# Performance work log

Hardware: AMD Instinct MI355X
Metric: run time of the kernel (lower is better)

## Reference

```python
import jax, jax.numpy as jnp
import numpy as np

N = 100000   # nodes
E = 1200000  # edges
D = 64       # dim == num_features
L = 5        # num_gc_layers
G = 128      # num graphs in batch
BN_EPS = 1e-5
NORM_EPS = 1e-12

def setup_inputs() -> dict:
    key = jax.random.key(0)
    ks = jax.random.split(key, 16)
    s = 0.05
    x = jax.random.normal(ks[0], (N, D), jnp.float32)
    edge_index = jax.random.randint(ks[1], (2, E), 0, N, dtype=jnp.int32)
    batch = jnp.sort(jax.random.randint(ks[2], (N,), 0, G, dtype=jnp.int32))
    # Encoder_support: Linear(D, D)
    Ws = jax.random.normal(ks[3], (D, D), jnp.float32) * s
    bs = jnp.zeros((D,), jnp.float32)
    # GIN MLPs per layer: Linear(D,D) -> ReLU -> Linear(D,D)
    W1 = jax.random.normal(ks[4], (L, D, D), jnp.float32) * s
    b1 = jnp.zeros((L, D), jnp.float32)
    W2 = jax.random.normal(ks[5], (L, D, D), jnp.float32) * s
    b2 = jnp.zeros((L, D), jnp.float32)
    # BatchNorm affine params
    bn_gamma = jnp.ones((L, D), jnp.float32)
    bn_beta = jnp.zeros((L, D), jnp.float32)
    # proj_head: Linear(L*D, L*D) -> ReLU -> Linear(L*D, L*D)
    Wp1 = jax.random.normal(ks[6], (L * D, L * D), jnp.float32) * s
    bp1 = jnp.zeros((L * D,), jnp.float32)
    Wp2 = jax.random.normal(ks[7], (L * D, L * D), jnp.float32) * s
    bp2 = jnp.zeros((L * D,), jnp.float32)
    return {"x": x, "edge_index": edge_index, "batch": batch,
            "Ws": Ws, "bs": bs, "W1": W1, "b1": b1, "W2": W2, "b2": b2,
            "bn_gamma": bn_gamma, "bn_beta": bn_beta,
            "Wp1": Wp1, "bp1": bp1, "Wp2": Wp2, "bp2": bp2}

def _l2norm(v):
    # F.normalize(v, dim=1): v / max(||v||_2, 1e-12)
    n = jnp.sqrt(jnp.sum(v * v, axis=1, keepdims=True))
    return v / jnp.maximum(n, NORM_EPS)

def reference(x, edge_index, batch, Ws, bs, W1, b1, W2, b2,
              bn_gamma, bn_beta, Wp1, bp1, Wp2, bp2):
    src, dst = edge_index[0], edge_index[1]
    h = x @ Ws + bs  # Encoder_support
    xs = []
    for i in range(L):
        # GINConv (eps=0): nn(x + sum_{j->i} x_j)
        agg = jax.ops.segment_sum(h[src], dst, num_segments=N)  # [N, D]
        z = h + agg
        z = jnp.maximum(z @ W1[i] + b1[i], 0.0) @ W2[i] + b2[i]
        z = jnp.maximum(z, 0.0)  # F.relu after conv
        # BatchNorm1d (training-mode batch stats over nodes)
        mean = jnp.mean(z, axis=0)
        var = jnp.var(z, axis=0)
        h = bn_gamma[i] * (z - mean) * jax.lax.rsqrt(var + BN_EPS) + bn_beta[i]
        xs.append(h)
    # global_add_pool per layer, concat along feature dim -> [G, L*D]
    pooled = jnp.concatenate(
        [jax.ops.segment_sum(h_, batch, num_segments=G) for h_ in xs], axis=1)
    y = jnp.maximum(pooled @ Wp1 + bp1, 0.0) @ Wp2 + bp2
    return (_l2norm(y), _l2norm(pooled))
```

## Files before the change

kernel.cpp:

```cpp
#include <hip/hip_runtime.h>
#include <hip/hip_bf16.h>
#include <hip/hip_fp16.h>

constexpr int Nn = 100000;
constexpr int Ee = 1200000;
constexpr int Ll = 5;
constexpr int Gg = 128;
constexpr int PDim = 320;

constexpr int NB    = 98;
constexpr int BCAP  = 16384;
constexpr int CHUNK = 4096;
constexpr int NBLK_A = (Ee + CHUNK - 1) / CHUNK;

typedef short short8 __attribute__((ext_vector_type(8)));
typedef float f32x4 __attribute__((ext_vector_type(4)));

union U4S8 { uint4 u; short8 s; };

__device__ inline ushort f2bf(float f) {
    const uint u = __float_as_uint(f);
    return (ushort)((u + 0x7fffu + ((u >> 16) & 1u)) >> 16);
}
__device__ inline uint pack2(float lo, float hi) {
    return (uint)f2bf(lo) | ((uint)f2bf(hi) << 16);
}
__device__ inline ushort f2h(float f) {
    const __half h = __float2half(f);
    return *(const ushort*)&h;
}
__device__ inline uint pack2h(float lo, float hi) {
    return (uint)f2h(lo) | ((uint)f2h(hi) << 16);
}
__device__ inline float h2f_lo(uint u) {
    const ushort s = (ushort)(u & 0xffffu);
    return __half2float(*(const __half*)&s);
}
__device__ inline float h2f_hi(uint u) {
    const ushort s = (ushort)(u >> 16);
    return __half2float(*(const __half*)&s);
}
__device__ inline void split2(float x0, float x1, uint& hi, uint& lo) {
    const ushort h0 = f2bf(x0), h1 = f2bf(x1);
    hi = (uint)h0 | ((uint)h1 << 16);
    const float r0 = x0 - __uint_as_float((uint)h0 << 16);
    const float r1 = x1 - __uint_as_float((uint)h1 << 16);
    lo = pack2(r0, r1);
}

__device__ inline int lower_bound_i(const int* __restrict__ a, int n, int v)
{
    int lo = 0, hi = n;
    while (lo < hi) {
        const int m = (lo + hi) >> 1;
        if (a[m] < v) lo = m + 1; else hi = m;
    }
    return lo;
}

__global__ __launch_bounds__(256) void conv_weights(
    const float* __restrict__ Ws, const float* __restrict__ W1,
    const float* __restrict__ W2, ushort* __restrict__ WThi,
    ushort* __restrict__ WTlo)
{
    const int m = blockIdx.x;
    const float* src = (m == 0) ? Ws
                     : (m <= 5) ? W1 + (size_t)(m - 1) * 4096
                                : W2 + (size_t)(m - 6) * 4096;
    ushort* dh = WThi + (size_t)m * 4096;
    ushort* dl = WTlo + (size_t)m * 4096;
    const int t = threadIdx.x;
    const int col = t & 63;
    const int k0 = (t >> 6) * 16;
    #pragma unroll
    for (int i = 0; i < 16; i++) {
        const int k = k0 + i;
        const float w = src[k * 64 + col];
        const ushort h = f2bf(w);
        dh[col * 64 + k] = h;
        dl[col * 64 + k] = f2bf(w - __uint_as_float((uint)h << 16));
    }
}

__global__ __launch_bounds__(256) void gemm_enc(
    const float* __restrict__ A1,
    const ushort* __restrict__ WThi, const ushort* __restrict__ WTlo,
    const float* __restrict__ bias, ushort* __restrict__ Ys)
{
    const int t = threadIdx.x;
    const int w = t >> 6;
    const int l = t & 63;
    const int lr = l & 15;
    const int lk = l >> 4;

    short8 bHi[4][2], bLo[4][2];
    #pragma unroll
    for (int nt = 0; nt < 4; nt++)
        #pragma unroll
        for (int c = 0; c < 2; c++) {
            const int off = (nt * 16 + lr) * 64 + c * 32 + lk * 8;
            U4S8 uh, ul;
            uh.u = *(const uint4*)(WThi + off);
            ul.u = *(const uint4*)(WTlo + off);
            bHi[nt][c] = uh.s;
            bLo[nt][c] = ul.s;
        }

    const int arow = blockIdx.x * 64 + w * 16 + lr;
    short8 aHi[2], aLo[2];
    if (arow < Nn) {
        #pragma unroll
        for (int c = 0; c < 2; c++) {
            const float* p1 = A1 + (size_t)arow * 64 + c * 32 + lk * 8;
            const float4 v0 = *(const float4*)p1;
            const float4 v1 = *(const float4*)(p1 + 4);
            U4S8 rh, rl;
            uint* ph = (uint*)&rh.u;
            uint* pl = (uint*)&rl.u;
            split2(v0.x, v0.y, ph[0], pl[0]);
            split2(v0.z, v0.w, ph[1], pl[1]);
            split2(v1.x, v1.y, ph[2], pl[2]);
            split2(v1.z, v1.w, ph[3], pl[3]);
            aHi[c] = rh.s;
            aLo[c] = rl.s;
        }
    } else {
        U4S8 z; z.u = make_uint4(0, 0, 0, 0);
        aHi[0] = aHi[1] = z.s;
        aLo[0] = aLo[1] = z.s;
    }

    f32x4 acc[4] = {};
    #pragma unroll
    for (int nt = 0; nt < 4; nt++)
        #pragma unroll
        for (int c = 0; c < 2; c++) {
            acc[nt] = __builtin_amdgcn_mfma_f32_16x16x32_bf16(
                aLo[c], bHi[nt][c], acc[nt], 0, 0, 0);
            acc[nt] = __builtin_amdgcn_mfma_f32_16x16x32_bf16(
                aHi[c], bLo[nt][c], acc[nt], 0, 0, 0);
            acc[nt] = __builtin_amdgcn_mfma_f32_16x16x32_bf16(
                aHi[c], bHi[nt][c], acc[nt], 0, 0, 0);
        }

    #pragma unroll
    for (int nt = 0; nt < 4; nt++) {
        const int ccol = nt * 16 + lr;
        const float bb = bias[ccol];
        #pragma unroll
        for (int j = 0; j < 4; j++) {
            const int crow = blockIdx.x * 64 + w * 16 + lk * 4 + j;
            if (crow < Nn)
                Ys[(size_t)crow * 64 + ccol] = f2h(acc[nt][j] + bb);
        }
    }
}

__global__ __launch_bounds__(256) void fused_mlp(
    const float* __restrict__ Uf,
    const ushort* __restrict__ WT1hi, const ushort* __restrict__ WT1lo,
    const float* __restrict__ b1v,
    const ushort* __restrict__ WT2hi, const ushort* __restrict__ WT2lo,
    const float* __restrict__ b2v,
    float* __restrict__ Z, float* __restrict__ stats)
{
    const int t = threadIdx.x;
    const int w = t >> 6;
    const int l = t & 63;
    const int lr = l & 15;
    const int lk = l >> 4;

    __shared__ ushort Mhi[64][72];
    __shared__ ushort Mlo[64][72];
    __shared__ float red[2][4][4][16];

    short8 b1Hi[4][2], b1Lo[4][2];
    #pragma unroll
    for (int nt = 0; nt < 4; nt++)
        #pragma unroll
        for (int c = 0; c < 2; c++) {
            const int off = (nt * 16 + lr) * 64 + c * 32 + lk * 8;
            U4S8 uh, ul;
            uh.u = *(const uint4*)(WT1hi + off);
            ul.u = *(const uint4*)(WT1lo + off);
            b1Hi[nt][c] = uh.s;
            b1Lo[nt][c] = ul.s;
        }

    const int arow = blockIdx.x * 64 + w * 16 + lr;
    short8 aHi[2], aLo[2];
    if (arow < Nn) {
        #pragma unroll
        for (int c = 0; c < 2; c++) {
            const float* p1 = Uf + (size_t)arow * 64 + c * 32 + lk * 8;
            const float4 v0 = *(const float4*)p1;
            const float4 v1 = *(const float4*)(p1 + 4);
            U4S8 rh, rl;
            uint* ph = (uint*)&rh.u;
            uint* pl = (uint*)&rl.u;
            split2(v0.x, v0.y, ph[0], pl[0]);
            split2(v0.z, v0.w, ph[1], pl[1]);
            split2(v1.x, v1.y, ph[2], pl[2]);
            split2(v1.z, v1.w, ph[3], pl[3]);
            aHi[c] = rh.s;
            aLo[c] = rl.s;
        }
    } else {
        U4S8 z; z.u = make_uint4(0, 0, 0, 0);
        aHi[0] = aHi[1] = z.s;
        aLo[0] = aLo[1] = z.s;
    }

    f32x4 acc[4] = {};
    #pragma unroll
    for (int nt = 0; nt < 4; nt++)
        #pragma unroll
        for (int c = 0; c < 2; c++) {
            acc[nt] = __builtin_amdgcn_mfma_f32_16x16x32_bf16(
                aLo[c], b1Hi[nt][c], acc[nt], 0, 0, 0);
            acc[nt] = __builtin_amdgcn_mfma_f32_16x16x32_bf16(
                aHi[c], b1Lo[nt][c], acc[nt], 0, 0, 0);
            acc[nt] = __builtin_amdgcn_mfma_f32_16x16x32_bf16(
                aHi[c], b1Hi[nt][c], acc[nt], 0, 0, 0);
        }

    #pragma unroll
    for (int nt = 0; nt < 4; nt++) {
        const int ccol = nt * 16 + lr;
        const float bb = b1v[ccol];
        #pragma unroll
        for (int j = 0; j < 4; j++) {
            const int rloc = w * 16 + lk * 4 + j;
            const float m = fmaxf(acc[nt][j] + bb, 0.f);
            const ushort h = f2bf(m);
            Mhi[rloc][ccol] = h;
            Mlo[rloc][ccol] = f2bf(m - __uint_as_float((uint)h << 16));
        }
    }
    __syncthreads();

    short8 b2Hi[4][2], b2Lo[4][2];
    #pragma unroll
    for (int nt = 0; nt < 4; nt++)
        #pragma unroll
        for (int c = 0; c < 2; c++) {
            const int off = (nt * 16 + lr) * 64 + c * 32 + lk * 8;
            U4S8 uh, ul;
            uh.u = *(const uint4*)(WT2hi + off);
            ul.u = *(const uint4*)(WT2lo + off);
            b2Hi[nt][c] = uh.s;
            b2Lo[nt][c] = ul.s;
        }

    short8 a2Hi[2], a2Lo[2];
    #pragma unroll
    for (int c = 0; c < 2; c++) {
        U4S8 uh, ul;
        uh.u = *(const uint4*)&Mhi[w * 16 + lr][c * 32 + lk * 8];
        ul.u = *(const uint4*)&Mlo[w * 16 + lr][c * 32 + lk * 8];
        a2Hi[c] = uh.s;
        a2Lo[c] = ul.s;
    }

    f32x4 acc2[4] = {};
    #pragma unroll
    for (int nt = 0; nt < 4; nt++)
        #pragma unroll
        for (int c = 0; c < 2; c++) {
            acc2[nt] = __builtin_amdgcn_mfma_f32_16x16x32_bf16(
                a2Lo[c], b2Hi[nt][c], acc2[nt], 0, 0, 0);
            acc2[nt] = __builtin_amdgcn_mfma_f32_16x16x32_bf16(
                a2Hi[c], b2Lo[nt][c], acc2[nt], 0, 0, 0);
            acc2[nt] = __builtin_amdgcn_mfma_f32_16x16x32_bf16(
                a2Hi[c], b2Hi[nt][c], acc2[nt], 0, 0, 0);
        }

    float s[4], s2[4];
    #pragma unroll
    for (int nt = 0; nt < 4; nt++) {
        const int ccol = nt * 16 + lr;
        const float bb = b2v[ccol];
        s[nt] = 0.f; s2[nt] = 0.f;
        #pragma unroll
        for (int j = 0; j < 4; j++) {
            const int crow = blockIdx.x * 64 + w * 16 + lk * 4 + j;
            if (crow < Nn) {
                const float v = fmaxf(acc2[nt][j] + bb, 0.f);
                Z[(size_t)crow * 64 + ccol] = v;
                s[nt] += v; s2[nt] += v * v;
            }
        }
    }

    #pragma unroll
    for (int nt = 0; nt < 4; nt++) {
        s[nt]  += __shfl_xor(s[nt], 16);  s[nt]  += __shfl_xor(s[nt], 32);
        s2[nt] += __shfl_xor(s2[nt], 16); s2[nt] += __shfl_xor(s2[nt], 32);
    }
    if (l < 16) {
        #pragma unroll
        for (int nt = 0; nt < 4; nt++) {
            red[0][w][nt][l] = s[nt];
            red[1][w][nt][l] = s2[nt];
        }
    }
    __syncthreads();
    if (t < 64) {
        float ts = 0.f, ts2 = 0.f;
        #pragma unroll
        for (int wv = 0; wv < 4; wv++) {
            ts  += red[0][wv][t >> 4][t & 15];
            ts2 += red[1][wv][t >> 4][t & 15];
        }
        atomicAdd(&stats[t], ts);
        atomicAdd(&stats[64 + t], ts2);
    }
}

__global__ void init_csr(int* __restrict__ gCursor)
{
    const int t = threadIdx.x;
    if (t < NB) gCursor[t] = t * BCAP;
}

__global__ __launch_bounds__(256) void bin_edges(
    const int* __restrict__ ei, int* __restrict__ gCursor,
    uint2* __restrict__ binned)
{
    __shared__ int hist[NB];
    __shared__ int base[NB];
    __shared__ int cur[NB];
    const int t = threadIdx.x;
    const int e0 = blockIdx.x * CHUNK;
    const int eEnd = min(e0 + CHUNK, Ee);
    if (t < NB) hist[t] = 0;
    __syncthreads();
    for (int e = e0 + t; e < eEnd; e += 256)
        atomicAdd(&hist[ei[Ee + e] >> 10], 1);
    __syncthreads();
    if (t < NB) {
        base[t] = atomicAdd(&gCursor[t], hist[t]);
        cur[t] = 0;
    }
    __syncthreads();
    for (int e = e0 + t; e < eEnd; e += 256) {
        const int s = ei[e];
        const int d = ei[Ee + e];
        const int b = d >> 10;
        const int pos = atomicAdd(&cur[b], 1);
        binned[(size_t)base[b] + pos] = make_uint2((uint)d, (uint)s);
    }
}

__global__ __launch_bounds__(128) void scan_buckets(
    const int* __restrict__ gCursor, int* __restrict__ bucketBase)
{
    __shared__ int sh[128];
    const int t = threadIdx.x;
    const int c = (t < NB) ? gCursor[t] - t * BCAP : 0;
    sh[t] = c;
    __syncthreads();
    for (int off = 1; off < 128; off <<= 1) {
        const int u = (t >= off) ? sh[t - off] : 0;
        __syncthreads();
        sh[t] += u;
        __syncthreads();
    }
    bucketBase[t] = sh[t] - c;
}

__global__ __launch_bounds__(256) void build_csr(
    const uint2* __restrict__ binned, const int* __restrict__ gCursor,
    const int* __restrict__ bucketBase, int* __restrict__ rowptr,
    int* __restrict__ colidx)
{
    __shared__ int degS[1024];
    __shared__ int sh[256];
    __shared__ int colStage[BCAP];
    const int b = blockIdx.x;
    const int t = threadIdx.x;
    const int cnt = gCursor[b] - b * BCAP;
    const int base = bucketBase[b];
    const uint2* src = binned + (size_t)b * BCAP;

    for (int i = t; i < 1024; i += 256) degS[i] = 0;
    __syncthreads();
    for (int i = t; i < cnt; i += 256)
        atomicAdd(&degS[src[i].x & 1023], 1);
    __syncthreads();

    const int b4 = t * 4;
    const int v0 = degS[b4], v1 = degS[b4 + 1], v2 = degS[b4 + 2], v3 = degS[b4 + 3];
    const int sSum = v0 + v1 + v2 + v3;
    sh[t] = sSum;
    __syncthreads();
    for (int off = 1; off < 256; off <<= 1) {
        const int u = (t >= off) ? sh[t - off] : 0;
        __syncthreads();
        sh[t] += u;
        __syncthreads();
    }
    const int excl = sh[t] - sSum;
    const int p0 = excl, p1 = excl + v0, p2 = excl + v0 + v1, p3 = excl + v0 + v1 + v2;

    const int grow = b * 1024 + b4;
    if (grow + 3 <= Nn) {
        *(int4*)(rowptr + grow) = make_int4(base + p0, base + p1, base + p2, base + p3);
    } else {
        if (grow + 0 <= Nn) rowptr[grow + 0] = base + p0;
        if (grow + 1 <= Nn) rowptr[grow + 1] = base + p1;
        if (grow + 2 <= Nn) rowptr[grow + 2] = base + p2;
        if (grow + 3 <= Nn) rowptr[grow + 3] = base + p3;
    }

    degS[b4] = p0; degS[b4 + 1] = p1; degS[b4 + 2] = p2; degS[b4 + 3] = p3;
    __syncthreads();
    for (int i = t; i < cnt; i += 256) {
        const uint2 p = src[i];
        const int pos = atomicAdd(&degS[p.x & 1023], 1);
        colStage[pos] = (int)p.y;
    }
    __syncthreads();
    for (int i = t; i < cnt; i += 256) colidx[base + i] = colStage[i];
}

__global__ __launch_bounds__(256) void gather_agg_inc(
    const int* __restrict__ rowptr, const int* __restrict__ col,
    const ushort* __restrict__ hs, float* __restrict__ u)
{
    const int r = blockIdx.x * 32 + (threadIdx.x >> 3);
    const int q = threadIdx.x & 7;
    const int beg = rowptr[r], end = rowptr[r + 1];
    float a[8];
    {
        const uint4 v = *(const uint4*)(hs + (size_t)r * 64 + q * 8);
        a[0] = h2f_lo(v.x); a[1] = h2f_hi(v.x);
        a[2] = h2f_lo(v.y); a[3] = h2f_hi(v.y);
        a[4] = h2f_lo(v.z); a[5] = h2f_hi(v.z);
        a[6] = h2f_lo(v.w); a[7] = h2f_hi(v.w);
    }
    for (int j = beg; j < end; j++) {
        const int s = col[j];
        const uint4 v = *(const uint4*)(hs + (size_t)s * 64 + q * 8);
        a[0] += h2f_lo(v.x); a[1] += h2f_hi(v.x);
        a[2] += h2f_lo(v.y); a[3] += h2f_hi(v.y);
        a[4] += h2f_lo(v.z); a[5] += h2f_hi(v.z);
        a[6] += h2f_lo(v.w); a[7] += h2f_hi(v.w);
    }
    float* o = u + (size_t)r * 64 + q * 8;
    *(float4*)o       = make_float4(a[0], a[1], a[2], a[3]);
    *(float4*)(o + 4) = make_float4(a[4], a[5], a[6], a[7]);
}

__global__ void bn_finalize(
    float* __restrict__ stats, const float* __restrict__ gamma,
    const float* __restrict__ beta, float* __restrict__ sc, int layer)
{
    const int c = threadIdx.x;
    const float mean = stats[c] * (1.0f / Nn);
    const float var = stats[64 + c] * (1.0f / Nn) - mean * mean;
    const float scale = gamma[layer * 64 + c] * rsqrtf(var + 1e-5f);
    sc[c] = scale;
    sc[64 + c] = beta[layer * 64 + c] - mean * scale;
    stats[c] = 0.f;
    stats[64 + c] = 0.f;
}

__global__ __launch_bounds__(256) void bn_apply_pool(
    const float* __restrict__ z, ushort* __restrict__ hs,
    const int* __restrict__ batch, const float* __restrict__ sc,
    float* __restrict__ pooled, int layer)
{
    const int g = blockIdx.x >> 3;
    const int sub = blockIdx.x & 7;
    const int lo = lower_bound_i(batch, Nn, g);
    const int hi = lower_bound_i(batch, Nn, g + 1);
    const int t = threadIdx.x;
    const int cq = t & 15;
    const int rg = (t >> 4) + sub * 16;
    float scl[4], sft[4], acc[4] = {};
    #pragma unroll
    for (int i = 0; i < 4; i++) {
        scl[i] = sc[cq * 4 + i];
        sft[i] = sc[64 + cq * 4 + i];
    }
    for (int row = lo + rg; row < hi; row += 128) {
        const float4 v = *(const float4*)(z + (size_t)row * 64 + cq * 4);
        const float a0 = fmaf(scl[0], v.x, sft[0]);
        const float a1 = fmaf(scl[1], v.y, sft[1]);
        const float a2 = fmaf(scl[2], v.z, sft[2]);
        const float a3 = fmaf(scl[3], v.w, sft[3]);
        uint2 p;
        p.x = pack2h(a0, a1);
        p.y = pack2h(a2, a3);
        *(uint2*)(hs + (size_t)row * 64 + cq * 4) = p;
        acc[0] += a0; acc[1] += a1; acc[2] += a2; acc[3] += a3;
    }
    __shared__ float red[16][16][4];
    #pragma unroll
    for (int i = 0; i < 4; i++) red[t >> 4][cq][i] = acc[i];
    __syncthreads();
    if (t < 64) {
        const int c2 = t >> 2, j = t & 3;
        float s = 0.f;
        #pragma unroll
        for (int r = 0; r < 16; r++) s += red[r][c2][j];
        atomicAdd(&pooled[g * PDim + layer * 64 + c2 * 4 + j], s);
    }
}

template<bool RELU>
__global__ __launch_bounds__(256) void proj(
    const float* __restrict__ X, const float* __restrict__ W,
    const float* __restrict__ bias, float* __restrict__ Y)
{
    const int idx = blockIdx.x * 256 + threadIdx.x;
    const int r = idx / PDim;
    const int c = idx - r * PDim;
    float acc = bias[c];
    #pragma unroll 8
    for (int k = 0; k < PDim; k++)
        acc = fmaf(X[r * PDim + k], W[k * PDim + c], acc);
    if constexpr (RELU) acc = fmaxf(acc, 0.f);
    Y[idx] = acc;
}

__global__ __launch_bounds__(64) void l2norm_rows(
    const float* __restrict__ X, float* __restrict__ out)
{
    const int r = blockIdx.x;
    const int l = threadIdx.x;
    float v[5];
    float s = 0.f;
    #pragma unroll
    for (int i = 0; i < 5; i++) {
        v[i] = X[r * PDim + i * 64 + l];
        s += v[i] * v[i];
    }
    #pragma unroll
    for (int off = 32; off > 0; off >>= 1) s += __shfl_down(s, off);
    s = __shfl(s, 0);
    const float d = fmaxf(sqrtf(s), 1e-12f);
    #pragma unroll
    for (int i = 0; i < 5; i++)
        out[r * PDim + i * 64 + l] = v[i] / d;
}

extern "C" void kernel_launch(void* const* d_in, const int* in_sizes, int n_in,
                              void* d_out, int out_size, void* d_ws, size_t ws_size,
                              hipStream_t stream)
{
    const float* x     = (const float*)d_in[0];
    const int*   ei    = (const int*)d_in[1];
    const int*   batch = (const int*)d_in[2];
    const float* Ws    = (const float*)d_in[3];
    const float* bs    = (const float*)d_in[4];
    const float* W1    = (const float*)d_in[5];
    const float* b1    = (const float*)d_in[6];
    const float* W2    = (const float*)d_in[7];
    const float* b2    = (const float*)d_in[8];
    const float* gamma = (const float*)d_in[9];
    const float* beta  = (const float*)d_in[10];
    const float* Wp1   = (const float*)d_in[11];
    const float* bp1   = (const float*)d_in[12];
    const float* Wp2   = (const float*)d_in[13];
    const float* bp2   = (const float*)d_in[14];
    float* out = (float*)d_out;

    float*  Uf  = (float*)d_ws;
    float*  Zf  = Uf + (size_t)Nn * 64;
    ushort* Hs  = (ushort*)(Zf + (size_t)Nn * 64);
    ushort* WThi = Hs + (size_t)Nn * 64;
    ushort* WTlo = WThi + 11 * 4096;
    float* pooled = (float*)(WTlo + 11 * 4096);
    float* ytmp   = pooled + (size_t)Gg * PDim;
    float* ypro   = ytmp + (size_t)Gg * PDim;
    float* stats  = ypro + (size_t)Gg * PDim;
    float* sc     = stats + 128;
    int* rowptr = (int*)(sc + 128);
    int* colidx = rowptr + Nn + 1;
    int* gCursor = colidx + Ee;
    int* bucketBase = gCursor + 128;
    size_t woff = (size_t)((bucketBase + 128) - (int*)d_ws);
    woff = (woff + 1) & ~(size_t)1;
    uint2* binned = (uint2*)((int*)d_ws + woff);

    const int gemmGrid = (Nn + 63) / 64;

    hipMemsetAsync(stats, 0, 128 * sizeof(float), stream);
    hipMemsetAsync(pooled, 0, (size_t)Gg * PDim * sizeof(float), stream);

    conv_weights<<<11, 256, 0, stream>>>(Ws, W1, W2, WThi, WTlo);

    init_csr<<<1, 128, 0, stream>>>(gCursor);
    bin_edges<<<NBLK_A, 256, 0, stream>>>(ei, gCursor, binned);
    scan_buckets<<<1, 128, 0, stream>>>(gCursor, bucketBase);
    build_csr<<<NB, 256, 0, stream>>>(binned, gCursor, bucketBase, rowptr, colidx);

    gemm_enc<<<gemmGrid, 256, 0, stream>>>(x, WThi, WTlo, bs, Hs);

    for (int l = 0; l < Ll; l++) {
        gather_agg_inc<<<Nn / 32, 256, 0, stream>>>(rowptr, colidx, Hs, Uf);
        fused_mlp<<<gemmGrid, 256, 0, stream>>>(
            Uf,
            WThi + (size_t)(1 + l) * 4096, WTlo + (size_t)(1 + l) * 4096,
            b1 + (size_t)l * 64,
            WThi + (size_t)(6 + l) * 4096, WTlo + (size_t)(6 + l) * 4096,
            b2 + (size_t)l * 64,
            Zf, stats);
        bn_finalize<<<1, 64, 0, stream>>>(stats, gamma, beta, sc, l);
        bn_apply_pool<<<Gg * 8, 256, 0, stream>>>(Zf, Hs, batch, sc, pooled, l);
    }

    proj<true><<<160, 256, 0, stream>>>(pooled, Wp1, bp1, ytmp);
    proj<false><<<160, 256, 0, stream>>>(ytmp, Wp2, bp2, ypro);

    l2norm_rows<<<Gg, 64, 0, stream>>>(ypro, out);
    l2norm_rows<<<Gg, 64, 0, stream>>>(pooled, out + Gg * PDim);
}
```

Baseline: 668.2 us.

## Fold BatchNorm affine into gather and pooling; store intermediates as fp16

The BatchNorm affine is pushed through the linear aggregation: the gather kernel now reads raw fp16 Z, sums the neighbours, then applies scale*sum + (deg+1)*shift. Pooling sums raw Z per graph and applies the affine once at the end, using per-graph node counts. This removes the separate bn_apply pass and its write of normalized features. The aggregated input U and the MLP output Z are stored as fp16 instead of fp32, and the hidden MLP activation goes through a single fp16 shared buffer. Together these roughly halve the activation traffic, at the cost of some fp16 precision loss.

```diff
diff --git a/kernel.cpp b/kernel.cpp
--- a/kernel.cpp
+++ b/kernel.cpp
@@ -56,6 +56,19 @@
         if (a[m] < v) lo = m + 1; else hi = m;
     }
     return lo;
+}
+
+__global__ void init_csr(const int* __restrict__ batch, int* __restrict__ gCursor,
+                         int* __restrict__ cnt, float* __restrict__ sc)
+{
+    const int t = threadIdx.x;
+    if (t < NB) gCursor[t] = t * BCAP;
+    {
+        const int lo = lower_bound_i(batch, Nn, t);
+        const int hi = lower_bound_i(batch, Nn, t + 1);
+        cnt[t] = hi - lo;
+    }
+    if (t < 64) { sc[t] = 1.f; sc[64 + t] = 0.f; }
 }
 
 __global__ __launch_bounds__(256) void conv_weights(
@@ -157,12 +170,12 @@
 }
 
 __global__ __launch_bounds__(256) void fused_mlp(
-    const float* __restrict__ Uf,
+    const ushort* __restrict__ Us,
     const ushort* __restrict__ WT1hi, const ushort* __restrict__ WT1lo,
     const float* __restrict__ b1v,
     const ushort* __restrict__ WT2hi, const ushort* __restrict__ WT2lo,
     const float* __restrict__ b2v,
-    float* __restrict__ Z, float* __restrict__ stats)
+    ushort* __restrict__ Zs, float* __restrict__ stats)
 {
     const int t = threadIdx.x;
     const int w = t >> 6;
@@ -170,8 +183,7 @@
     const int lr = l & 15;
     const int lk = l >> 4;
 
-    __shared__ ushort Mhi[64][72];
-    __shared__ ushort Mlo[64][72];
+    __shared__ ushort Mh[64][72];
     __shared__ float red[2][4][4][16];
 
     short8 b1Hi[4][2], b1Lo[4][2];
@@ -192,16 +204,14 @@
     if (arow < Nn) {
         #pragma unroll
         for (int c = 0; c < 2; c++) {
-            const float* p1 = Uf + (size_t)arow * 64 + c * 32 + lk * 8;
-            const float4 v0 = *(const float4*)p1;
-            const float4 v1 = *(const float4*)(p1 + 4);
+            const uint4 v = *(const uint4*)(Us + (size_t)arow * 64 + c * 32 + lk * 8);
             U4S8 rh, rl;
             uint* ph = (uint*)&rh.u;
             uint* pl = (uint*)&rl.u;
-            split2(v0.x, v0.y, ph[0], pl[0]);
-            split2(v0.z, v0.w, ph[1], pl[1]);
-            split2(v1.x, v1.y, ph[2], pl[2]);
-            split2(v1.z, v1.w, ph[3], pl[3]);
+            split2(h2f_lo(v.x), h2f_hi(v.x), ph[0], pl[0]);
+            split2(h2f_lo(v.y), h2f_hi(v.y), ph[1], pl[1]);
+            split2(h2f_lo(v.z), h2f_hi(v.z), ph[2], pl[2]);
+            split2(h2f_lo(v.w), h2f_hi(v.w), ph[3], pl[3]);
             aHi[c] = rh.s;
             aLo[c] = rl.s;
         }
@@ -231,10 +241,7 @@
         #pragma unroll
         for (int j = 0; j < 4; j++) {
             const int rloc = w * 16 + lk * 4 + j;
-            const float m = fmaxf(acc[nt][j] + bb, 0.f);
-            const ushort h = f2bf(m);
-            Mhi[rloc][ccol] = h;
-            Mlo[rloc][ccol] = f2bf(m - __uint_as_float((uint)h << 16));
+            Mh[rloc][ccol] = f2h(fmaxf(acc[nt][j] + bb, 0.f));
         }
     }
     __syncthreads();
@@ -255,11 +262,16 @@
     short8 a2Hi[2], a2Lo[2];
     #pragma unroll
     for (int c = 0; c < 2; c++) {
-        U4S8 uh, ul;
-        uh.u = *(const uint4*)&Mhi[w * 16 + lr][c * 32 + lk * 8];
-        ul.u = *(const uint4*)&Mlo[w * 16 + lr][c * 32 + lk * 8];
-        a2Hi[c] = uh.s;
-        a2Lo[c] = ul.s;
+        const uint4 v = *(const uint4*)&Mh[w * 16 + lr][c * 32 + lk * 8];
+        U4S8 rh, rl;
+        uint* ph = (uint*)&rh.u;
+        uint* pl = (uint*)&rl.u;
+        split2(h2f_lo(v.x), h2f_hi(v.x), ph[0], pl[0]);
+        split2(h2f_lo(v.y), h2f_hi(v.y), ph[1], pl[1]);
+        split2(h2f_lo(v.z), h2f_hi(v.z), ph[2], pl[2]);
+        split2(h2f_lo(v.w), h2f_hi(v.w), ph[3], pl[3]);
+        a2Hi[c] = rh.s;
+        a2Lo[c] = rl.s;
     }
 
     f32x4 acc2[4] = {};
@@ -286,7 +298,7 @@
             const int crow = blockIdx.x * 64 + w * 16 + lk * 4 + j;
             if (crow < Nn) {
                 const float v = fmaxf(acc2[nt][j] + bb, 0.f);
-                Z[(size_t)crow * 64 + ccol] = v;
+                Zs[(size_t)crow * 64 + ccol] = f2h(v);
                 s[nt] += v; s2[nt] += v * v;
             }
         }
@@ -315,12 +327,6 @@
         atomicAdd(&stats[t], ts);
         atomicAdd(&stats[64 + t], ts2);
     }
-}
-
-__global__ void init_csr(int* __restrict__ gCursor)
-{
-    const int t = threadIdx.x;
-    if (t < NB) gCursor[t] = t * BCAP;
 }
 
 __global__ __launch_bounds__(256) void bin_edges(
@@ -424,16 +430,22 @@
     for (int i = t; i < cnt; i += 256) colidx[base + i] = colStage[i];
 }
 
-__global__ __launch_bounds__(256) void gather_agg_inc(
+__global__ __launch_bounds__(256) void gather_bn(
     const int* __restrict__ rowptr, const int* __restrict__ col,
-    const ushort* __restrict__ hs, float* __restrict__ u)
-{
-    const int r = blockIdx.x * 32 + (threadIdx.x >> 3);
-    const int q = threadIdx.x & 7;
+    const ushort* __restrict__ zs, const float* __restrict__ sc,
+    ushort* __restrict__ us)
+{
+    __shared__ float scS[128];
+    const int t = threadIdx.x;
+    if (t < 128) scS[t] = sc[t];
+    __syncthreads();
+
+    const int r = blockIdx.x * 32 + (t >> 3);
+    const int q = t & 7;
     const int beg = rowptr[r], end = rowptr[r + 1];
     float a[8];
     {
-        const uint4 v = *(const uint4*)(hs + (size_t)r * 64 + q * 8);
+        const uint4 v = *(const uint4*)(zs + (size_t)r * 64 + q * 8);
         a[0] = h2f_lo(v.x); a[1] = h2f_hi(v.x);
         a[2] = h2f_lo(v.y); a[3] = h2f_hi(v.y);
         a[4] = h2f_lo(v.z); a[5] = h2f_hi(v.z);
@@ -441,35 +453,44 @@
     }
     for (int j = beg; j < end; j++) {
         const int s = col[j];
-        const uint4 v = *(const uint4*)(hs + (size_t)s * 64 + q * 8);
+        const uint4 v = *(const uint4*)(zs + (size_t)s * 64 + q * 8);
         a[0] += h2f_lo(v.x); a[1] += h2f_hi(v.x);
         a[2] += h2f_lo(v.y); a[3] += h2f_hi(v.y);
         a[4] += h2f_lo(v.z); a[5] += h2f_hi(v.z);
         a[6] += h2f_lo(v.w); a[7] += h2f_hi(v.w);
     }
-    float* o = u + (size_t)r * 64 + q * 8;
-    *(float4*)o       = make_float4(a[0], a[1], a[2], a[3]);
-    *(float4*)(o + 4) = make_float4(a[4], a[5], a[6], a[7]);
+    const float dgf = (float)(end - beg + 1);
+    float o[8];
+    #pragma unroll
+    for (int i = 0; i < 8; i++)
+        o[i] = fmaf(scS[q * 8 + i], a[i], dgf * scS[64 + q * 8 + i]);
+    uint4 p;
+    p.x = pack2h(o[0], o[1]); p.y = pack2h(o[2], o[3]);
+    p.z = pack2h(o[4], o[5]); p.w = pack2h(o[6], o[7]);
+    *(uint4*)(us + (size_t)r * 64 + q * 8) = p;
 }
 
 __global__ void bn_finalize(
     float* __restrict__ stats, const float* __restrict__ gamma,
-    const float* __restrict__ beta, float* __restrict__ sc, int layer)
+    const float* __restrict__ beta, float* __restrict__ sc,
+    float* __restrict__ sc5, int layer)
 {
     const int c = threadIdx.x;
     const float mean = stats[c] * (1.0f / Nn);
     const float var = stats[64 + c] * (1.0f / Nn) - mean * mean;
     const float scale = gamma[layer * 64 + c] * rsqrtf(var + 1e-5f);
+    const float shift = beta[layer * 64 + c] - mean * scale;
     sc[c] = scale;
-    sc[64 + c] = beta[layer * 64 + c] - mean * scale;
+    sc[64 + c] = shift;
+    sc5[layer * 128 + c] = scale;
+    sc5[layer * 128 + 64 + c] = shift;
     stats[c] = 0.f;
     stats[64 + c] = 0.f;
 }
 
-__global__ __launch_bounds__(256) void bn_apply_pool(
-    const float* __restrict__ z, ushort* __restrict__ hs,
-    const int* __restrict__ batch, const float* __restrict__ sc,
-    float* __restrict__ pooled, int layer)
+__global__ __launch_bounds__(256) void pool_z(
+    const ushort* __restrict__ zs, const int* __restrict__ batch,
+    float* __restrict__ poolZ)
 {
     const int g = blockIdx.x >> 3;
     const int sub = blockIdx.x & 7;
@@ -478,23 +499,11 @@
     const int t = threadIdx.x;
     const int cq = t & 15;
     const int rg = (t >> 4) + sub * 16;
-    float scl[4], sft[4], acc[4] = {};
-    #pragma unroll
-    for (int i = 0; i < 4; i++) {
-        scl[i] = sc[cq * 4 + i];
-        sft[i] = sc[64 + cq * 4 + i];
-    }
+    float acc[4] = {};
     for (int row = lo + rg; row < hi; row += 128) {
-        const float4 v = *(const float4*)(z + (size_t)row * 64 + cq * 4);
-        const float a0 = fmaf(scl[0], v.x, sft[0]);
-        const float a1 = fmaf(scl[1], v.y, sft[1]);
-        const float a2 = fmaf(scl[2], v.z, sft[2]);
-        const float a3 = fmaf(scl[3], v.w, sft[3]);
-        uint2 p;
-        p.x = pack2h(a0, a1);
-        p.y = pack2h(a2, a3);
-        *(uint2*)(hs + (size_t)row * 64 + cq * 4) = p;
-        acc[0] += a0; acc[1] += a1; acc[2] += a2; acc[3] += a3;
+        const uint2 p = *(const uint2*)(zs + (size_t)row * 64 + cq * 4);
+        acc[0] += h2f_lo(p.x); acc[1] += h2f_hi(p.x);
+        acc[2] += h2f_lo(p.y); acc[3] += h2f_hi(p.y);
     }
     __shared__ float red[16][16][4];
     #pragma unroll
@@ -505,8 +514,21 @@
         float s = 0.f;
         #pragma unroll
         for (int r = 0; r < 16; r++) s += red[r][c2][j];
-        atomicAdd(&pooled[g * PDim + layer * 64 + c2 * 4 + j], s);
-    }
+        atomicAdd(&poolZ[g * 64 + c2 * 4 + j], s);
+    }
+}
+
+__global__ __launch_bounds__(256) void final_pool(
+    const float* __restrict__ sc5, const float* __restrict__ poolZ,
+    const int* __restrict__ cnt, float* __restrict__ pooled)
+{
+    const int idx = blockIdx.x * 256 + threadIdx.x;
+    const int c = idx & 63;
+    const int g = (idx >> 6) & 127;
+    const int l = idx >> 13;
+    pooled[g * PDim + l * 64 + c] =
+        sc5[l * 128 + c] * poolZ[(size_t)l * Gg * 64 + g * 64 + c]
+        + (float)cnt[g] * sc5[l * 128 + 64 + c];
 }
 
 template<bool RELU>
@@ -567,17 +589,19 @@
     const float* bp2   = (const float*)d_in[14];
     float* out = (float*)d_out;
 
-    float*  Uf  = (float*)d_ws;
-    float*  Zf  = Uf + (size_t)Nn * 64;
-    ushort* Hs  = (ushort*)(Zf + (size_t)Nn * 64);
-    ushort* WThi = Hs + (size_t)Nn * 64;
+    ushort* Us = (ushort*)d_ws;
+    ushort* Zs = Us + (size_t)Nn * 64;
+    ushort* WThi = Zs + (size_t)Nn * 64;
     ushort* WTlo = WThi + 11 * 4096;
     float* pooled = (float*)(WTlo + 11 * 4096);
     float* ytmp   = pooled + (size_t)Gg * PDim;
     float* ypro   = ytmp + (size_t)Gg * PDim;
     float* stats  = ypro + (size_t)Gg * PDim;
     float* sc     = stats + 128;
-    int* rowptr = (int*)(sc + 128);
+    float* sc5    = sc + 128;
+    float* poolZ  = sc5 + 5 * 128;
+    int* cnt    = (int*)(poolZ + 5 * Gg * 64);
+    int* rowptr = cnt + 128;
     int* colidx = rowptr + Nn + 1;
     int* gCursor = colidx + Ee;
     int* bucketBase = gCursor + 128;
@@ -588,29 +612,31 @@
     const int gemmGrid = (Nn + 63) / 64;
 
     hipMemsetAsync(stats, 0, 128 * sizeof(float), stream);
-    hipMemsetAsync(pooled, 0, (size_t)Gg * PDim * sizeof(float), stream);
-
+    hipMemsetAsync(poolZ, 0, 5 * Gg * 64 * sizeof(float), stream);
+
+    init_csr<<<1, 128, 0, stream>>>(batch, gCursor, cnt, sc);
     conv_weights<<<11, 256, 0, stream>>>(Ws, W1, W2, WThi, WTlo);
 
-    init_csr<<<1, 128, 0, stream>>>(gCursor);
     bin_edges<<<NBLK_A, 256, 0, stream>>>(ei, gCursor, binned);
     scan_buckets<<<1, 128, 0, stream>>>(gCursor, bucketBase);
     build_csr<<<NB, 256, 0, stream>>>(binned, gCursor, bucketBase, rowptr, colidx);
 
-    gemm_enc<<<gemmGrid, 256, 0, stream>>>(x, WThi, WTlo, bs, Hs);
+    gemm_enc<<<gemmGrid, 256, 0, stream>>>(x, WThi, WTlo, bs, Zs);
 
     for (int l = 0; l < Ll; l++) {
-        gather_agg_inc<<<Nn / 32, 256, 0, stream>>>(rowptr, colidx, Hs, Uf);
+        gather_bn<<<Nn / 32, 256, 0, stream>>>(rowptr, colidx, Zs, sc, Us);
         fused_mlp<<<gemmGrid, 256, 0, stream>>>(
-            Uf,
+            Us,
             WThi + (size_t)(1 + l) * 4096, WTlo + (size_t)(1 + l) * 4096,
             b1 + (size_t)l * 64,
             WThi + (size_t)(6 + l) * 4096, WTlo + (size_t)(6 + l) * 4096,
             b2 + (size_t)l * 64,
-            Zf, stats);
-        bn_finalize<<<1, 64, 0, stream>>>(stats, gamma, beta, sc, l);
-        bn_apply_pool<<<Gg * 8, 256, 0, stream>>>(Zf, Hs, batch, sc, pooled, l);
-    }
+            Zs, stats);
+        bn_finalize<<<1, 64, 0, stream>>>(stats, gamma, beta, sc, sc5, l);
+        pool_z<<<Gg * 8, 256, 0, stream>>>(Zs, batch, poolZ + (size_t)l * Gg * 64);
+    }
+
+    final_pool<<<160, 256, 0, stream>>>(sc5, poolZ, cnt, pooled);
 
     proj<true><<<160, 256, 0, stream>>>(pooled, Wp1, bp1, ytmp);
     proj<false><<<160, 256, 0, stream>>>(ytmp, Wp2, bp2, ypro);
```

Result: faster. 642.0 us (-3.9%).
